# Optimization experiments

Measured on AMD Instinct MI355X. Metric: run time of the kernel, lower is better.

Reference implementation:

```python
import jax, jax.numpy as jnp
import numpy as np

B, C_IN, C_OUT, H, W = 8, 32, 32, 512, 512
HM0, HM1 = 16, 16  # half_modes = n_modes // 2
FFT_NORM = 'backward'
SCALE = 1.0 / (C_IN * C_OUT)  # scale='auto'


def setup_inputs() -> dict:
    key = jax.random.key(0)
    ks = jax.random.split(key, 6)
    x = jax.random.normal(ks[0], (B, C_IN, H, W), jnp.float32)
    # two corner weights (2**(order-1) * n_layers = 2), stored as real/imag parts
    w1r = SCALE * jax.random.normal(ks[1], (C_IN, C_OUT, HM0, HM1), jnp.float32)
    w1i = SCALE * jax.random.normal(ks[2], (C_IN, C_OUT, HM0, HM1), jnp.float32)
    w2r = SCALE * jax.random.normal(ks[3], (C_IN, C_OUT, HM0, HM1), jnp.float32)
    w2i = SCALE * jax.random.normal(ks[4], (C_IN, C_OUT, HM0, HM1), jnp.float32)
    bias = SCALE * jax.random.normal(ks[5], (C_OUT, 1, 1), jnp.float32)  # bias[indices=0]
    return {"x": x, "w1r": w1r, "w1i": w1i, "w2r": w2r, "w2i": w2i, "bias": bias}


def reference(x, w1r, w1i, w2r, w2i, bias):
    # rfftn over the spatial dims
    x_ft = jnp.fft.rfftn(x, axes=(-2, -1), norm=FFT_NORM)  # (B, C_IN, H, W//2+1) complex64
    w1 = w1r + 1j * w1i
    w2 = w2r + 1j * w2i
    # mode truncation + dense complex contraction per corner: 'bixy,ioxy->boxy'
    top = jnp.einsum('bixy,ioxy->boxy', x_ft[:, :, :HM0, :HM1], w1)
    bot = jnp.einsum('bixy,ioxy->boxy', x_ft[:, :, H - HM0:, :HM1], w2)
    out_ft = jnp.zeros((B, C_OUT, H, W // 2 + 1), dtype=x_ft.dtype)
    out_ft = out_ft.at[:, :, :HM0, :HM1].set(top)
    out_ft = out_ft.at[:, :, H - HM0:, :HM1].set(bot)
    y = jnp.fft.irfftn(out_ft, s=(H, W), axes=(-2, -1), norm=FFT_NORM)
    return y + bias  # bias broadcasts over (B, C_OUT, H, W)
```

## Files before the change

kernel.cpp:

```cpp
#include <hip/hip_runtime.h>
#include <math.h>

#define Hh 512
#define Ww 512
#define Bb 8
#define CI 32
#define CO 32
#define HM 16
#define KYp 32

static constexpr float TWO_PI = 6.28318530717958647692f;

#define F_OFF  4194304u
#define g_OFF  4718592u

using short8 = __attribute__((ext_vector_type(8))) short;
using f32x16 = __attribute__((ext_vector_type(16))) float;
using f32x4  = __attribute__((ext_vector_type(4))) float;

__device__ inline unsigned short bf16_rn(float f) {
  unsigned u = __float_as_uint(f);
  u += 0x7FFFu + ((u >> 16) & 1u);
  return (unsigned short)(u >> 16);
}

__device__ inline void split4(float4 v, uint2& h2, uint2& l2) {
  unsigned u0 = __float_as_uint(v.x), u1 = __float_as_uint(v.y);
  unsigned u2 = __float_as_uint(v.z), u3 = __float_as_uint(v.w);
  float f0 = v.x - __uint_as_float(u0 & 0xFFFF0000u);
  float f1 = v.y - __uint_as_float(u1 & 0xFFFF0000u);
  float f2 = v.z - __uint_as_float(u2 & 0xFFFF0000u);
  float f3 = v.w - __uint_as_float(u3 & 0xFFFF0000u);
  h2.x = (u1 & 0xFFFF0000u) | (u0 >> 16);
  h2.y = (u3 & 0xFFFF0000u) | (u2 >> 16);
  l2.x = (__float_as_uint(f1) & 0xFFFF0000u) | (__float_as_uint(f0) >> 16);
  l2.y = (__float_as_uint(f3) & 0xFFFF0000u) | (__float_as_uint(f2) >> 16);
}

__global__ __launch_bounds__(256) void e_init_kernel(float* __restrict__ Ef) {
  unsigned short* E = (unsigned short*)Ef;
  int idx = blockIdx.x * 256 + threadIdx.x;
  if (idx < 16384) {
    int kk = idx >> 9;
    int l = (idx >> 3) & 63;
    int j = idx & 7;
    int k = kk * 16 + 8 * (l >> 5) + j;
    int col = l & 31;
    int kx = col >> 1;
    int t = (kx * k) & 511;
    float sv, cv;
    sincosf(TWO_PI * (float)t / 512.0f, &sv, &cv);
    E[idx] = bf16_rn((col & 1) ? -sv : cv);
  } else if (idx < 49152) {
    int idx2 = idx - 16384;
    int mt = idx2 >> 14;
    int rem = idx2 & 16383;
    int kk = rem >> 9;
    int l = (rem >> 3) & 63;
    int j = rem & 7;
    int h = kk * 16 + 8 * (l >> 5) + j;
    int kyc = l & 31;
    int kyp = mt * 16 + (kyc >> 1);
    int ky = (kyp < 16) ? kyp : (kyp + 480);
    int t = (ky * h) & 511;
    float sv, cv;
    sincosf(TWO_PI * (float)t / 512.0f, &sv, &cv);
    E[idx] = bf16_rn((kyc & 1) ? -sv : cv);
  } else {
    int rem = idx - 49152;
    int ntile = rem >> 10;
    int s = (rem >> 9) & 1;
    int l = (rem >> 3) & 63;
    int j = rem & 7;
    int K = s * 16 + 8 * (l >> 5) + j;
    int k = K >> 1, c = K & 1;
    int w = ntile * 32 + (l & 31);
    int t = (k * w) & 511;
    float sv, cv;
    sincosf(TWO_PI * (float)t / 512.0f, &sv, &cv);
    float wk = (k == 0) ? 1.0f : 2.0f;
    float inv = 1.0f / 262144.0f;
    E[idx] = bf16_rn(inv * wk * (c ? -sv : cv));
  }
}

__global__ __launch_bounds__(512) void fwd_kernel(const float* __restrict__ x,
                                                  const float* __restrict__ Ef,
                                                  const float* __restrict__ E2f,
                                                  float* __restrict__ F) {
  __shared__ char lds[135168];
  short* E2l = (short*)lds;
  short* Xh  = (short*)(lds + 65536);
  short* Xl  = (short*)(lds + 98304);
  float* red = (float*)(lds + 65536);
  short* Ah  = (short*)(lds + 131072);
  short* Al  = (short*)(lds + 133120);
  float* Pbuf = (float*)(lds + 65536);

  const int tid = threadIdx.x;
  const int l = tid & 63;
  const int wid = tid >> 6;
  const int bi = blockIdx.x;
  const float* xb = x + (size_t)bi * (Hh * Ww);

  {
    const float4* Eg = (const float4*)E2f;
    float4* El4 = (float4*)E2l;
    #pragma unroll
    for (int j = 0; j < 8; ++j) El4[tid + j * 512] = Eg[tid + j * 512];
  }
  short8 e1[4];
  {
    const short* Eg = (const short*)Ef;
    #pragma unroll
    for (int c = 0; c < 4; ++c)
      e1[c] = *(const short8*)(Eg + ((size_t)(4 * wid + c) * 64 + l) * 8);
  }

  const int hb = (l >> 1) & 1;
  const int jfr = 4 * (l & 1);
  const int kc0 = l >> 2;

  float4 rv[8];
  #pragma unroll
  for (int j = 0; j < 4; ++j) {
    const float* rowp = xb + (size_t)(wid * 4 + j) * 512;
    rv[2 * j]     = *(const float4*)(rowp + 4 * l);
    rv[2 * j + 1] = *(const float4*)(rowp + 256 + 4 * l);
  }

  f32x16 acc1 = {0.f,0.f,0.f,0.f,0.f,0.f,0.f,0.f,0.f,0.f,0.f,0.f,0.f,0.f,0.f,0.f};
  f32x16 acc2 = {0.f,0.f,0.f,0.f,0.f,0.f,0.f,0.f,0.f,0.f,0.f,0.f,0.f,0.f,0.f,0.f};

  const int mt2 = wid & 1, kc2w = (wid >> 1) & 1, part2 = wid >> 2;

  for (int s = 0; s < 16; ++s) {
    if (s > 0) {
      short8 a2 = *(const short8*)&E2l[((mt2 * 32 + ((s - 1) * 2 + kc2w)) * 64 + l) * 8];
      short8 b2 = part2 ? *(const short8*)&Al[(kc2w * 64 + l) * 8]
                        : *(const short8*)&Ah[(kc2w * 64 + l) * 8];
      acc2 = __builtin_amdgcn_mfma_f32_32x32x16_bf16(a2, b2, acc2, 0, 0, 0);
    }
    #pragma unroll
    for (int j = 0; j < 4; ++j) {
      #pragma unroll
      for (int hf = 0; hf < 2; ++hf) {
        int kc = hf * 16 + kc0;
        int lanep = (wid * 4 + j) + 32 * hb;
        int off = ((kc * 64) + (lanep ^ (kc & 7))) * 8 + jfr;
        uint2 h2, l2;
        split4(rv[2 * j + hf], h2, l2);
        *(uint2*)&Xh[off] = h2;
        *(uint2*)&Xl[off] = l2;
      }
    }
    if (s < 15) {
      #pragma unroll
      for (int j = 0; j < 4; ++j) {
        const float* rowp = xb + (size_t)((s + 1) * 32 + wid * 4 + j) * 512;
        rv[2 * j]     = *(const float4*)(rowp + 4 * l);
        rv[2 * j + 1] = *(const float4*)(rowp + 256 + 4 * l);
      }
    }
    __syncthreads();
    #pragma unroll
    for (int c = 0; c < 4; ++c) {
      int kc = 4 * wid + c;
      int slot = ((kc * 64) + (l ^ (kc & 7))) * 8;
      short8 hi = *(const short8*)&Xh[slot];
      short8 lo = *(const short8*)&Xl[slot];
      acc1 = __builtin_amdgcn_mfma_f32_32x32x16_bf16(hi, e1[c], acc1, 0, 0, 0);
      acc1 = __builtin_amdgcn_mfma_f32_32x32x16_bf16(lo, e1[c], acc1, 0, 0, 0);
    }
    __syncthreads();
    #pragma unroll
    for (int q = 0; q < 4; ++q)
      *(float4*)&red[((wid * 4 + q) * 64 + l) * 4] =
          make_float4(acc1[4*q], acc1[4*q+1], acc1[4*q+2], acc1[4*q+3]);
    #pragma unroll
    for (int r = 0; r < 16; ++r) acc1[r] = 0.f;
    __syncthreads();
    if (wid < 4) {
      const int q = wid;
      float4 sum = make_float4(0.f, 0.f, 0.f, 0.f);
      #pragma unroll
      for (int w = 0; w < 8; ++w) {
        float4 v = *(const float4*)&red[((w * 4 + q) * 64 + l) * 4];
        sum.x += v.x; sum.y += v.y; sum.z += v.z; sum.w += v.w;
      }
      uint2 h2, l2;
      split4(sum, h2, l2);
      int off = ((q >> 1) * 64 + ((l & 31) + 32 * (q & 1))) * 8 + 4 * (l >> 5);
      *(uint2*)&Ah[off] = h2;
      *(uint2*)&Al[off] = l2;
    }
    __syncthreads();
  }
  {
    short8 a2 = *(const short8*)&E2l[((mt2 * 32 + (15 * 2 + kc2w)) * 64 + l) * 8];
    short8 b2 = part2 ? *(const short8*)&Al[(kc2w * 64 + l) * 8]
                      : *(const short8*)&Ah[(kc2w * 64 + l) * 8];
    acc2 = __builtin_amdgcn_mfma_f32_32x32x16_bf16(a2, b2, acc2, 0, 0, 0);
  }
  #pragma unroll
  for (int r4 = 0; r4 < 4; ++r4)
    *(float4*)&Pbuf[((wid * 4 + r4) * 64 + l) * 4] =
        make_float4(acc2[4*r4], acc2[4*r4+1], acc2[4*r4+2], acc2[4*r4+3]);
  __syncthreads();

  if (wid < 2) {
    const int mt = wid;
    float S[16];
    #pragma unroll
    for (int r = 0; r < 16; ++r) S[r] = 0.f;
    #pragma unroll
    for (int p = 0; p < 4; ++p) {
      #pragma unroll
      for (int r4 = 0; r4 < 4; ++r4) {
        float4 v = *(const float4*)&Pbuf[(((mt + 2 * p) * 4 + r4) * 64 + l) * 4];
        S[4*r4]   += v.x; S[4*r4+1] += v.y; S[4*r4+2] += v.z; S[4*r4+3] += v.w;
      }
    }
    const int c = l & 1;
    #pragma unroll
    for (int q = 0; q < 8; ++q) {
      int r0 = 2 * q;
      float T = __shfl_xor(S[r0 + 1], 1, 64);
      float val = c ? (S[r0] + T) : (S[r0] - T);
      int kyp_loc = ((r0 & 3) >> 1) + 4 * (r0 >> 2) + 2 * (l >> 5);
      F[((size_t)bi * 32 + mt * 16 + kyp_loc) * 32 + (l & 31)] = val;
    }
  }
}

__global__ __launch_bounds__(512, 4) void bwd_kernel(const float* __restrict__ F,
    const float* __restrict__ w1r, const float* __restrict__ w1i,
    const float* __restrict__ w2r, const float* __restrict__ w2i,
    const float* __restrict__ bias, const float* __restrict__ T2f,
    float* __restrict__ y) {
  __shared__ char lds[73728];
  short* Ah   = (short*)lds;
  short* Al   = (short*)(lds + 16384);
  float* Gs   = (float*)(lds + 32768);
  float* ct   = (float*)(lds + 36864);
  float* st   = (float*)(lds + 38912);
  float* ybuf = (float*)(lds + 40960);

  const int tid = threadIdx.x;
  const int l = tid & 63;
  const int wid = tid >> 6;
  const int bo = blockIdx.x >> 1;
  const int half = blockIdx.x & 1;
  const int b = bo >> 5;
  const int o = bo & 31;
  const float bv = bias[o];

  short8 bfr[4];
  {
    const short* Tg = (const short*)T2f;
    #pragma unroll
    for (int q = 0; q < 4; ++q) {
      int nt = wid * 2 + (q >> 1);
      int s = q & 1;
      bfr[q] = *(const short8*)(Tg + ((size_t)(nt * 2 + s) * 64 + l) * 8);
    }
  }
  {
    float sv, cv;
    sincosf(TWO_PI * (float)tid / 512.0f, &sv, &cv);
    ct[tid] = cv;
    st[tid] = sv;
  }

  {
    const int kyp = tid >> 4;
    const int kx = tid & 15;
    const bool top = kyp < 16;
    const int m = top ? kyp : (kyp - 16);
    const float* wr = top ? w1r : w2r;
    const float* wi = top ? w1i : w2i;
    float gr = 0.f, gi = 0.f;
    for (int i = 0; i < CI; ++i) {
      float2 f = *(const float2*)&F[(((size_t)b * CI + i) * KYp + kyp) * (HM * 2) + kx * 2];
      size_t wo = (((size_t)i * CO + o) * HM + m) * HM + kx;
      float wrv = wr[wo], wiv = wi[wo];
      gr = fmaf(f.x, wrv, gr); gr = fmaf(-f.y, wiv, gr);
      gi = fmaf(f.x, wiv, gi); gi = fmaf(f.y, wrv, gi);
    }
    Gs[(kyp * HM + kx) * 2]     = gr;
    Gs[(kyp * HM + kx) * 2 + 1] = gi;
  }
  __syncthreads();

  {
    const int r = tid & 255;
    const int h = half * 256 + r;
    const int kxh = tid >> 8;
    float gr[8], gi[8];
    #pragma unroll
    for (int k = 0; k < 8; ++k) { gr[k] = 0.f; gi[k] = 0.f; }
    #pragma unroll 4
    for (int kyp = 0; kyp < 32; ++kyp) {
      const int ky = (kyp < 16) ? kyp : (kyp + 480);
      const int t = (ky * h) & 511;
      const float cc = ct[t], ss = st[t];
      float4 row[4];
      #pragma unroll
      for (int j = 0; j < 4; ++j) row[j] = *(const float4*)&Gs[kyp * 32 + kxh * 16 + j * 4];
      #pragma unroll
      for (int k = 0; k < 8; ++k) {
        float Gr = ((const float*)row)[2 * k];
        float Gi = ((const float*)row)[2 * k + 1];
        gr[k] = fmaf(Gr, cc, gr[k]); gr[k] = fmaf(-Gi, ss, gr[k]);
        gi[k] = fmaf(Gr, ss, gi[k]); gi[k] = fmaf(Gi, cc, gi[k]);
      }
    }
    const int mt_loc = r >> 5;
    const int rr = r & 31;
    const int s = kxh;
    #pragma unroll
    for (int hf2 = 0; hf2 < 2; ++hf2) {
      int k0 = hf2 * 4;
      float4 va = make_float4(gr[k0], gi[k0], gr[k0 + 1], gi[k0 + 1]);
      float4 vb = make_float4(gr[k0 + 2], gi[k0 + 2], gr[k0 + 3], gi[k0 + 3]);
      uint2 ha, la, hb, lb;
      split4(va, ha, la);
      split4(vb, hb, lb);
      int off = ((mt_loc * 2 + s) * 64 + rr + 32 * hf2) * 8;
      *(uint4*)&Ah[off] = make_uint4(ha.x, ha.y, hb.x, hb.y);
      *(uint4*)&Al[off] = make_uint4(la.x, la.y, lb.x, lb.y);
    }
  }
  __syncthreads();

  {
    float* yb = y + (size_t)bo * (Hh * Ww) + (size_t)half * 256 * Ww;
    const int colA = (wid * 2) * 32 + (l & 31);
    const int colB = (wid * 2 + 1) * 32 + (l & 31);
    const int rq = 4 * (l >> 5);
    for (int mt = 0; mt < 8; ++mt) {
      short8 a_h0 = *(const short8*)&Ah[((mt * 2 + 0) * 64 + l) * 8];
      short8 a_l0 = *(const short8*)&Al[((mt * 2 + 0) * 64 + l) * 8];
      short8 a_h1 = *(const short8*)&Ah[((mt * 2 + 1) * 64 + l) * 8];
      short8 a_l1 = *(const short8*)&Al[((mt * 2 + 1) * 64 + l) * 8];
      f32x16 accA, accB;
      #pragma unroll
      for (int r = 0; r < 16; ++r) { accA[r] = bv; accB[r] = bv; }
      accA = __builtin_amdgcn_mfma_f32_32x32x16_bf16(a_h0, bfr[0], accA, 0, 0, 0);
      accA = __builtin_amdgcn_mfma_f32_32x32x16_bf16(a_l0, bfr[0], accA, 0, 0, 0);
      accA = __builtin_amdgcn_mfma_f32_32x32x16_bf16(a_h1, bfr[1], accA, 0, 0, 0);
      accA = __builtin_amdgcn_mfma_f32_32x32x16_bf16(a_l1, bfr[1], accA, 0, 0, 0);
      accB = __builtin_amdgcn_mfma_f32_32x32x16_bf16(a_h0, bfr[2], accB, 0, 0, 0);
      accB = __builtin_amdgcn_mfma_f32_32x32x16_bf16(a_l0, bfr[2], accB, 0, 0, 0);
      accB = __builtin_amdgcn_mfma_f32_32x32x16_bf16(a_h1, bfr[3], accB, 0, 0, 0);
      accB = __builtin_amdgcn_mfma_f32_32x32x16_bf16(a_l1, bfr[3], accB, 0, 0, 0);
      #pragma unroll
      for (int hf = 0; hf < 2; ++hf) {
        #pragma unroll
        for (int rr = 0; rr < 8; ++rr) {
          int r = 8 * hf + rr;
          int row = (r & 3) + 8 * ((r >> 2) & 1) + rq;
          ybuf[row * 512 + colA] = accA[r];
          ybuf[row * 512 + colB] = accB[r];
        }
        asm volatile("s_waitcnt lgkmcnt(0)\n\ts_barrier" ::: "memory");
        {
          const f32x4* yb4 = (const f32x4*)ybuf;
          float* ybase = yb + (size_t)(mt * 32 + hf * 16) * 512;
          #pragma unroll
          for (int j = 0; j < 4; ++j) {
            int f4 = tid + j * 512;
            f32x4* dst = (f32x4*)(ybase + (size_t)(f4 >> 7) * 512 + (f4 & 127) * 4);
            __builtin_nontemporal_store(yb4[f4], dst);
          }
        }
        asm volatile("s_waitcnt lgkmcnt(0)\n\ts_barrier" ::: "memory");
      }
    }
  }
}

extern "C" void kernel_launch(void* const* d_in, const int* in_sizes, int n_in,
                              void* d_out, int out_size, void* d_ws, size_t ws_size,
                              hipStream_t stream) {
  const float* x    = (const float*)d_in[0];
  const float* w1r  = (const float*)d_in[1];
  const float* w1i  = (const float*)d_in[2];
  const float* w2r  = (const float*)d_in[3];
  const float* w2i  = (const float*)d_in[4];
  const float* bias = (const float*)d_in[5];
  float* y  = (float*)d_out;
  float* ws = (float*)d_ws;
  float* F   = ws + F_OFF;
  float* E   = ws + g_OFF;
  float* E2c = ws + g_OFF + 8192;
  float* T2f = ws + g_OFF + 24576;

  hipLaunchKernelGGL(e_init_kernel, dim3(256), dim3(256), 0, stream, E);
  hipLaunchKernelGGL(fwd_kernel, dim3(Bb * CI), dim3(512), 0, stream, x, E, E2c, F);
  hipLaunchKernelGGL(bwd_kernel, dim3(Bb * CO * 2), dim3(512), 0, stream, F,
                     w1r, w1i, w2r, w2i, bias, T2f, y);
}
```

Baseline: 114.6 us.

## Split channel mixing into its own kernel and spread backward pass over more blocks

The per-(b,o) spectral channel contraction moves out of the backward kernel into a separate mix_kernel that writes G to workspace. This stops it from being recomputed by every half-block. The backward kernel now splits each output image into 8 row chunks of 64 instead of 2 halves, giving 2048 blocks with a smaller LDS footprint and a higher occupancy hint. Each thread does less inverse-DFT work. The cost is an extra kernel launch, a global round trip for G, and repeated twiddle and B-fragment setup in more blocks.

```diff
diff --git a/kernel.cpp b/kernel.cpp
--- a/kernel.cpp
+++ b/kernel.cpp
@@ -12,6 +12,7 @@
 static constexpr float TWO_PI = 6.28318530717958647692f;
 
 #define F_OFF  4194304u
+#define G_OFF  4456448u
 #define g_OFF  4718592u
 
 using short8 = __attribute__((ext_vector_type(8))) short;
@@ -233,25 +234,47 @@
   }
 }
 
-__global__ __launch_bounds__(512, 4) void bwd_kernel(const float* __restrict__ F,
+__global__ __launch_bounds__(512) void mix_kernel(const float* __restrict__ F,
     const float* __restrict__ w1r, const float* __restrict__ w1i,
     const float* __restrict__ w2r, const float* __restrict__ w2i,
+    float* __restrict__ G) {
+  const int tid = threadIdx.x;
+  const int b = blockIdx.x >> 5;
+  const int o = blockIdx.x & 31;
+  const int kyp = tid >> 4;
+  const int kx = tid & 15;
+  const bool top = kyp < 16;
+  const int m = top ? kyp : (kyp - 16);
+  const float* wr = top ? w1r : w2r;
+  const float* wi = top ? w1i : w2i;
+  float gr = 0.f, gi = 0.f;
+  for (int i = 0; i < CI; ++i) {
+    float2 f = *(const float2*)&F[(((size_t)b * CI + i) * KYp + kyp) * (HM * 2) + kx * 2];
+    size_t wo = (((size_t)i * CO + o) * HM + m) * HM + kx;
+    float wrv = wr[wo], wiv = wi[wo];
+    gr = fmaf(f.x, wrv, gr); gr = fmaf(-f.y, wiv, gr);
+    gi = fmaf(f.x, wiv, gi); gi = fmaf(f.y, wrv, gi);
+  }
+  size_t go = ((size_t)blockIdx.x * KYp + kyp) * (HM * 2) + kx * 2;
+  *(float2*)(G + go) = make_float2(gr, gi);
+}
+
+__global__ __launch_bounds__(512, 6) void bwd_kernel(const float* __restrict__ G,
     const float* __restrict__ bias, const float* __restrict__ T2f,
     float* __restrict__ y) {
-  __shared__ char lds[73728];
+  __shared__ char lds[49152];
   short* Ah   = (short*)lds;
-  short* Al   = (short*)(lds + 16384);
-  float* Gs   = (float*)(lds + 32768);
-  float* ct   = (float*)(lds + 36864);
-  float* st   = (float*)(lds + 38912);
-  float* ybuf = (float*)(lds + 40960);
+  short* Al   = (short*)(lds + 4096);
+  float* Gs   = (float*)(lds + 8192);
+  float* ct   = (float*)(lds + 12288);
+  float* st   = (float*)(lds + 14336);
+  float* ybuf = (float*)(lds + 16384);
 
   const int tid = threadIdx.x;
   const int l = tid & 63;
   const int wid = tid >> 6;
-  const int bo = blockIdx.x >> 1;
-  const int half = blockIdx.x & 1;
-  const int b = bo >> 5;
+  const int bo = blockIdx.x >> 3;
+  const int chunk = blockIdx.x & 7;
   const int o = bo & 31;
   const float bv = bias[o];
 
@@ -270,75 +293,51 @@
     sincosf(TWO_PI * (float)tid / 512.0f, &sv, &cv);
     ct[tid] = cv;
     st[tid] = sv;
-  }
-
-  {
-    const int kyp = tid >> 4;
-    const int kx = tid & 15;
-    const bool top = kyp < 16;
-    const int m = top ? kyp : (kyp - 16);
-    const float* wr = top ? w1r : w2r;
-    const float* wi = top ? w1i : w2i;
-    float gr = 0.f, gi = 0.f;
-    for (int i = 0; i < CI; ++i) {
-      float2 f = *(const float2*)&F[(((size_t)b * CI + i) * KYp + kyp) * (HM * 2) + kx * 2];
-      size_t wo = (((size_t)i * CO + o) * HM + m) * HM + kx;
-      float wrv = wr[wo], wiv = wi[wo];
-      gr = fmaf(f.x, wrv, gr); gr = fmaf(-f.y, wiv, gr);
-      gi = fmaf(f.x, wiv, gi); gi = fmaf(f.y, wrv, gi);
-    }
-    Gs[(kyp * HM + kx) * 2]     = gr;
-    Gs[(kyp * HM + kx) * 2 + 1] = gi;
+    if (tid < 256)
+      ((float4*)Gs)[tid] = ((const float4*)(G + (size_t)bo * (KYp * HM * 2)))[tid];
   }
   __syncthreads();
 
   {
-    const int r = tid & 255;
-    const int h = half * 256 + r;
-    const int kxh = tid >> 8;
-    float gr[8], gi[8];
-    #pragma unroll
-    for (int k = 0; k < 8; ++k) { gr[k] = 0.f; gi[k] = 0.f; }
+    const int r = l;
+    const int h = chunk * 64 + r;
+    const int kxh = wid;
+    float gr[2], gi[2];
+    gr[0] = gr[1] = gi[0] = gi[1] = 0.f;
     #pragma unroll 4
     for (int kyp = 0; kyp < 32; ++kyp) {
       const int ky = (kyp < 16) ? kyp : (kyp + 480);
       const int t = (ky * h) & 511;
       const float cc = ct[t], ss = st[t];
-      float4 row[4];
-      #pragma unroll
-      for (int j = 0; j < 4; ++j) row[j] = *(const float4*)&Gs[kyp * 32 + kxh * 16 + j * 4];
-      #pragma unroll
-      for (int k = 0; k < 8; ++k) {
-        float Gr = ((const float*)row)[2 * k];
-        float Gi = ((const float*)row)[2 * k + 1];
+      float4 gv = *(const float4*)&Gs[kyp * 32 + kxh * 4];
+      #pragma unroll
+      for (int k = 0; k < 2; ++k) {
+        float Gr = ((const float*)&gv)[2 * k];
+        float Gi = ((const float*)&gv)[2 * k + 1];
         gr[k] = fmaf(Gr, cc, gr[k]); gr[k] = fmaf(-Gi, ss, gr[k]);
         gi[k] = fmaf(Gr, ss, gi[k]); gi[k] = fmaf(Gi, cc, gi[k]);
       }
     }
     const int mt_loc = r >> 5;
     const int rr = r & 31;
-    const int s = kxh;
-    #pragma unroll
-    for (int hf2 = 0; hf2 < 2; ++hf2) {
-      int k0 = hf2 * 4;
-      float4 va = make_float4(gr[k0], gi[k0], gr[k0 + 1], gi[k0 + 1]);
-      float4 vb = make_float4(gr[k0 + 2], gi[k0 + 2], gr[k0 + 3], gi[k0 + 3]);
-      uint2 ha, la, hb, lb;
-      split4(va, ha, la);
-      split4(vb, hb, lb);
-      int off = ((mt_loc * 2 + s) * 64 + rr + 32 * hf2) * 8;
-      *(uint4*)&Ah[off] = make_uint4(ha.x, ha.y, hb.x, hb.y);
-      *(uint4*)&Al[off] = make_uint4(la.x, la.y, lb.x, lb.y);
-    }
+    const int s = kxh >> 2;
+    const int halfk = (kxh >> 1) & 1;
+    const int j0 = 4 * (kxh & 1);
+    float4 va = make_float4(gr[0], gi[0], gr[1], gi[1]);
+    uint2 ha, la;
+    split4(va, ha, la);
+    int off = ((mt_loc * 2 + s) * 64 + rr + 32 * halfk) * 8 + j0;
+    *(uint2*)&Ah[off] = ha;
+    *(uint2*)&Al[off] = la;
   }
   __syncthreads();
 
   {
-    float* yb = y + (size_t)bo * (Hh * Ww) + (size_t)half * 256 * Ww;
+    float* yb = y + (size_t)bo * (Hh * Ww) + (size_t)chunk * 64 * Ww;
     const int colA = (wid * 2) * 32 + (l & 31);
     const int colB = (wid * 2 + 1) * 32 + (l & 31);
     const int rq = 4 * (l >> 5);
-    for (int mt = 0; mt < 8; ++mt) {
+    for (int mt = 0; mt < 2; ++mt) {
       short8 a_h0 = *(const short8*)&Ah[((mt * 2 + 0) * 64 + l) * 8];
       short8 a_l0 = *(const short8*)&Al[((mt * 2 + 0) * 64 + l) * 8];
       short8 a_h1 = *(const short8*)&Ah[((mt * 2 + 1) * 64 + l) * 8];
@@ -392,12 +391,15 @@
   float* y  = (float*)d_out;
   float* ws = (float*)d_ws;
   float* F   = ws + F_OFF;
+  float* G   = ws + G_OFF;
   float* E   = ws + g_OFF;
   float* E2c = ws + g_OFF + 8192;
   float* T2f = ws + g_OFF + 24576;
 
   hipLaunchKernelGGL(e_init_kernel, dim3(256), dim3(256), 0, stream, E);
   hipLaunchKernelGGL(fwd_kernel, dim3(Bb * CI), dim3(512), 0, stream, x, E, E2c, F);
-  hipLaunchKernelGGL(bwd_kernel, dim3(Bb * CO * 2), dim3(512), 0, stream, F,
-                     w1r, w1i, w2r, w2i, bias, T2f, y);
-}
+  hipLaunchKernelGGL(mix_kernel, dim3(Bb * CO), dim3(512), 0, stream, F,
+                     w1r, w1i, w2r, w2i, G);
+  hipLaunchKernelGGL(bwd_kernel, dim3(Bb * CO * 8), dim3(512), 0, stream, G,
+                     bias, T2f, y);
+}
```

Result: no change. 113.1 us (-1.3%).

## Split spectral channel mixing into its own kernel and store output directly

Applied to the files above, without the earlier changes.

Moves the complex weight contraction out of bwd_kernel into a separate mix_kernel that writes G to workspace. Each bwd block now loads its precomputed modes instead of recomputing them, so the two half-blocks no longer both redo the mixing. The LDS staging buffer for coalesced output writes is dropped in favour of direct scalar nontemporal stores from the MFMA accumulators. This shrinks LDS use from 72 KB to 40 KB, allowing more resident blocks, and removes barriers, at the cost of less coalesced global stores and an extra kernel launch.

```diff
diff --git a/kernel.cpp b/kernel.cpp
--- a/kernel.cpp
+++ b/kernel.cpp
@@ -12,6 +12,7 @@
 static constexpr float TWO_PI = 6.28318530717958647692f;
 
 #define F_OFF  4194304u
+#define G_OFF  4456448u
 #define g_OFF  4718592u
 
 using short8 = __attribute__((ext_vector_type(8))) short;
@@ -233,25 +234,46 @@
   }
 }
 
-__global__ __launch_bounds__(512, 4) void bwd_kernel(const float* __restrict__ F,
+__global__ __launch_bounds__(512) void mix_kernel(const float* __restrict__ F,
     const float* __restrict__ w1r, const float* __restrict__ w1i,
     const float* __restrict__ w2r, const float* __restrict__ w2i,
+    float* __restrict__ G) {
+  const int tid = threadIdx.x;
+  const int b = blockIdx.x >> 5;
+  const int o = blockIdx.x & 31;
+  const int kyp = tid >> 4;
+  const int kx = tid & 15;
+  const bool top = kyp < 16;
+  const int m = top ? kyp : (kyp - 16);
+  const float* wr = top ? w1r : w2r;
+  const float* wi = top ? w1i : w2i;
+  float gr = 0.f, gi = 0.f;
+  for (int i = 0; i < CI; ++i) {
+    float2 f = *(const float2*)&F[(((size_t)b * CI + i) * KYp + kyp) * (HM * 2) + kx * 2];
+    size_t wo = (((size_t)i * CO + o) * HM + m) * HM + kx;
+    float wrv = wr[wo], wiv = wi[wo];
+    gr = fmaf(f.x, wrv, gr); gr = fmaf(-f.y, wiv, gr);
+    gi = fmaf(f.x, wiv, gi); gi = fmaf(f.y, wrv, gi);
+  }
+  size_t go = ((size_t)blockIdx.x * KYp + kyp) * (HM * 2) + kx * 2;
+  *(float2*)(G + go) = make_float2(gr, gi);
+}
+
+__global__ __launch_bounds__(512, 4) void bwd_kernel(const float* __restrict__ G,
     const float* __restrict__ bias, const float* __restrict__ T2f,
     float* __restrict__ y) {
-  __shared__ char lds[73728];
+  __shared__ char lds[40960];
   short* Ah   = (short*)lds;
   short* Al   = (short*)(lds + 16384);
   float* Gs   = (float*)(lds + 32768);
   float* ct   = (float*)(lds + 36864);
   float* st   = (float*)(lds + 38912);
-  float* ybuf = (float*)(lds + 40960);
 
   const int tid = threadIdx.x;
   const int l = tid & 63;
   const int wid = tid >> 6;
   const int bo = blockIdx.x >> 1;
   const int half = blockIdx.x & 1;
-  const int b = bo >> 5;
   const int o = bo & 31;
   const float bv = bias[o];
 
@@ -270,25 +292,8 @@
     sincosf(TWO_PI * (float)tid / 512.0f, &sv, &cv);
     ct[tid] = cv;
     st[tid] = sv;
-  }
-
-  {
-    const int kyp = tid >> 4;
-    const int kx = tid & 15;
-    const bool top = kyp < 16;
-    const int m = top ? kyp : (kyp - 16);
-    const float* wr = top ? w1r : w2r;
-    const float* wi = top ? w1i : w2i;
-    float gr = 0.f, gi = 0.f;
-    for (int i = 0; i < CI; ++i) {
-      float2 f = *(const float2*)&F[(((size_t)b * CI + i) * KYp + kyp) * (HM * 2) + kx * 2];
-      size_t wo = (((size_t)i * CO + o) * HM + m) * HM + kx;
-      float wrv = wr[wo], wiv = wi[wo];
-      gr = fmaf(f.x, wrv, gr); gr = fmaf(-f.y, wiv, gr);
-      gi = fmaf(f.x, wiv, gi); gi = fmaf(f.y, wrv, gi);
-    }
-    Gs[(kyp * HM + kx) * 2]     = gr;
-    Gs[(kyp * HM + kx) * 2 + 1] = gi;
+    if (tid < 256)
+      ((float4*)Gs)[tid] = ((const float4*)(G + (size_t)bo * (KYp * HM * 2)))[tid];
   }
   __syncthreads();
 
@@ -355,26 +360,10 @@
       accB = __builtin_amdgcn_mfma_f32_32x32x16_bf16(a_h1, bfr[3], accB, 0, 0, 0);
       accB = __builtin_amdgcn_mfma_f32_32x32x16_bf16(a_l1, bfr[3], accB, 0, 0, 0);
       #pragma unroll
-      for (int hf = 0; hf < 2; ++hf) {
-        #pragma unroll
-        for (int rr = 0; rr < 8; ++rr) {
-          int r = 8 * hf + rr;
-          int row = (r & 3) + 8 * ((r >> 2) & 1) + rq;
-          ybuf[row * 512 + colA] = accA[r];
-          ybuf[row * 512 + colB] = accB[r];
-        }
-        asm volatile("s_waitcnt lgkmcnt(0)\n\ts_barrier" ::: "memory");
-        {
-          const f32x4* yb4 = (const f32x4*)ybuf;
-          float* ybase = yb + (size_t)(mt * 32 + hf * 16) * 512;
-          #pragma unroll
-          for (int j = 0; j < 4; ++j) {
-            int f4 = tid + j * 512;
-            f32x4* dst = (f32x4*)(ybase + (size_t)(f4 >> 7) * 512 + (f4 & 127) * 4);
-            __builtin_nontemporal_store(yb4[f4], dst);
-          }
-        }
-        asm volatile("s_waitcnt lgkmcnt(0)\n\ts_barrier" ::: "memory");
+      for (int r = 0; r < 16; ++r) {
+        int row = mt * 32 + (r & 3) + 8 * (r >> 2) + rq;
+        __builtin_nontemporal_store(accA[r], &yb[(size_t)row * Ww + colA]);
+        __builtin_nontemporal_store(accB[r], &yb[(size_t)row * Ww + colB]);
       }
     }
   }
@@ -392,12 +381,15 @@
   float* y  = (float*)d_out;
   float* ws = (float*)d_ws;
   float* F   = ws + F_OFF;
+  float* G   = ws + G_OFF;
   float* E   = ws + g_OFF;
   float* E2c = ws + g_OFF + 8192;
   float* T2f = ws + g_OFF + 24576;
 
   hipLaunchKernelGGL(e_init_kernel, dim3(256), dim3(256), 0, stream, E);
   hipLaunchKernelGGL(fwd_kernel, dim3(Bb * CI), dim3(512), 0, stream, x, E, E2c, F);
-  hipLaunchKernelGGL(bwd_kernel, dim3(Bb * CO * 2), dim3(512), 0, stream, F,
-                     w1r, w1i, w2r, w2i, bias, T2f, y);
-}
+  hipLaunchKernelGGL(mix_kernel, dim3(Bb * CO), dim3(512), 0, stream, F,
+                     w1r, w1i, w2r, w2i, G);
+  hipLaunchKernelGGL(bwd_kernel, dim3(Bb * CO * 2), dim3(512), 0, stream, G,
+                     bias, T2f, y);
+}
```

After: 117.4 us. 1.02x slower.
